# Performance work log

Hardware: AMD Instinct MI355X
Metric: run time of the kernel (lower is better)

Reference implementation:

```python
import jax, jax.numpy as jnp
import numpy as np

BATCH = 4096
FEATURES = 64
VOCAB = 580000
EMB_DIM = 32
MODELS = 512
SEQ_LEN = 128


def _positional_encoding(position, d_model):
    # Faithful to the numpy get_angles: 1/10000^(2*(i//2)/d_model), sin on even, cos on odd.
    pos = jnp.arange(position, dtype=jnp.float32)[:, None]          # [P, 1]
    i = jnp.arange(d_model, dtype=jnp.float32)[None, :]             # [1, D]
    angle_rates = 1.0 / jnp.power(10000.0, (2.0 * jnp.floor(i / 2.0)) / jnp.float32(d_model))
    angles = pos * angle_rates                                      # [P, D]
    even = (jnp.arange(d_model) % 2 == 0)[None, :]
    pe = jnp.where(even, jnp.sin(angles), jnp.cos(angles))
    return pe[None]                                                 # [1, P, D]


def setup_inputs() -> dict:
    key = jax.random.key(0)
    k1, k2, k3 = jax.random.split(key, 3)
    tokens = jax.random.randint(k1, (BATCH, FEATURES), 0, VOCAB, dtype=jnp.int32)
    emb_table = jax.random.normal(k2, (VOCAB, EMB_DIM), dtype=jnp.float32)
    W = jax.random.normal(k3, (FEATURES * EMB_DIM, MODELS), dtype=jnp.float32) * 0.02
    b = jnp.zeros((MODELS,), dtype=jnp.float32)
    return {"tokens": tokens, "emb_table": emb_table, "W": W, "b": b}


def reference(tokens, emb_table, W, b):
    B, F = tokens.shape
    # gather + scale by sqrt(models)
    x = emb_table[tokens] * jnp.sqrt(jnp.float32(MODELS))           # [B, F, E]
    x = x.reshape(B, F * EMB_DIM)                                   # [B, F*E]
    x = x @ W + b                                                   # [B, M]
    # tf.tile(row, [seq_len]) then reshape (seq_len, models) == broadcast over seq axis
    pe = _positional_encoding(SEQ_LEN, MODELS)                      # [1, S, M]
    out = x[:, None, :] + pe[:, :SEQ_LEN, :]                        # [B, S, M]
    return out
```

## Files before the change

### kernel.cpp

```cpp
#include <hip/hip_runtime.h>
#include <math.h>

#define BATCH   4096
#define FEAT    64
#define EMB     32
#define MODELS  512
#define SEQ     128
#define KDIM    (FEAT * EMB)

#define SQRT_MODELS 22.62741699796952f
#define LN10000     9.210340371976184f

typedef __attribute__((ext_vector_type(4))) float    f32x4;
typedef __attribute__((ext_vector_type(8))) short    bf16x8;
typedef __attribute__((ext_vector_type(4))) unsigned int u32x4;

#define WT_BYTES ((size_t)MODELS * KDIM * 2)
#define PE_BYTES ((size_t)SEQ * MODELS * 4)
#define X_BYTES  ((size_t)BATCH * MODELS * 4)
#define WS_NEEDED (WT_BYTES + PE_BYTES + X_BYTES)

__device__ inline unsigned short bf16_rne(float f) {
    unsigned int b = __builtin_bit_cast(unsigned int, f);
    return (unsigned short)((b + 0x7FFFu + ((b >> 16) & 1u)) >> 16);
}

__global__ __launch_bounds__(256)
void prep_wt(const float* __restrict__ W, unsigned short* __restrict__ Wt) {
    __shared__ float t[32][33];
    const int k0 = blockIdx.x * 32;
    const int n0 = blockIdx.y * 32;
    const int tx = threadIdx.x;
    const int ty = threadIdx.y;
    #pragma unroll
    for (int i = 0; i < 4; ++i) {
        const int kk = ty + i * 8;
        t[kk][tx] = W[(size_t)(k0 + kk) * MODELS + n0 + tx] * SQRT_MODELS;
    }
    __syncthreads();
    #pragma unroll
    for (int i = 0; i < 4; ++i) {
        const int nn = ty + i * 8;
        Wt[(size_t)(n0 + nn) * KDIM + k0 + tx] = bf16_rne(t[tx][nn]);
    }
}

__global__ __launch_bounds__(256)
void prep_pe(const float* __restrict__ bias, float* __restrict__ pe) {
    const int idx = blockIdx.x * 256 + threadIdx.x;
    const int s = idx >> 9;
    const int m = idx & (MODELS - 1);
    const float rate = expf(-LN10000 * (float)(2 * (m >> 1)) * (1.0f / 512.0f));
    const float ang  = (float)s * rate;
    pe[idx] = ((m & 1) ? cosf(ang) : sinf(ang)) + bias[m];
}

__global__ __launch_bounds__(256)
void gemm_mfma(const int* __restrict__ tokens, const float* __restrict__ emb,
               const unsigned short* __restrict__ Wt, float* __restrict__ x) {
    const int tid  = threadIdx.x;
    const int wave = tid >> 6;
    const int lane = tid & 63;
    const int ln   = lane & 15;
    const int kg   = lane >> 4;

    const int m_base = blockIdx.y * 16;
    const int n_base = blockIdx.x * 256 + wave * 64;

    const int* trow = tokens + (size_t)(m_base + ln) * FEAT;

    const unsigned short* bptr[4];
    #pragma unroll
    for (int nf = 0; nf < 4; ++nf)
        bptr[nf] = Wt + (size_t)(n_base + nf * 16 + ln) * KDIM + kg * 8;

    f32x4 acc[4] = {f32x4{0,0,0,0}, f32x4{0,0,0,0}, f32x4{0,0,0,0}, f32x4{0,0,0,0}};

    for (int f4 = 0; f4 < FEAT; f4 += 4) {
        const int4 tok4 = *(const int4*)(trow + f4);
        const int toks[4] = {tok4.x, tok4.y, tok4.z, tok4.w};
        #pragma unroll
        for (int j = 0; j < 4; ++j) {
            const int f = f4 + j;
            const float* ea = emb + (size_t)toks[j] * EMB + kg * 8;
            const f32x4 a0 = *(const f32x4*)ea;
            const f32x4 a1 = *(const f32x4*)(ea + 4);
            unsigned int q0, q1, q2, q3;
            asm("v_cvt_pk_bf16_f32 %0, %1, %2" : "=v"(q0) : "v"(a0.x), "v"(a0.y));
            asm("v_cvt_pk_bf16_f32 %0, %1, %2" : "=v"(q1) : "v"(a0.z), "v"(a0.w));
            asm("v_cvt_pk_bf16_f32 %0, %1, %2" : "=v"(q2) : "v"(a1.x), "v"(a1.y));
            asm("v_cvt_pk_bf16_f32 %0, %1, %2" : "=v"(q3) : "v"(a1.z), "v"(a1.w));
            const u32x4 pk = {q0, q1, q2, q3};
            const bf16x8 afrag = __builtin_bit_cast(bf16x8, pk);
            #pragma unroll
            for (int nf = 0; nf < 4; ++nf) {
                const bf16x8 bfrag = *(const bf16x8*)(bptr[nf] + (size_t)f * EMB);
                acc[nf] = __builtin_amdgcn_mfma_f32_16x16x32_bf16(afrag, bfrag, acc[nf], 0, 0, 0);
            }
        }
    }

    #pragma unroll
    for (int nf = 0; nf < 4; ++nf) {
        #pragma unroll
        for (int q = 0; q < 4; ++q) {
            const int r = kg * 4 + q;
            x[(size_t)(m_base + r) * MODELS + n_base + nf * 16 + ln] = acc[nf][q];
        }
    }
}

__global__ __launch_bounds__(256)
void bcast_pe(const float* __restrict__ x, const float* __restrict__ pe,
              float* __restrict__ out) {
    const int tid = threadIdx.x;
    const int m4  = tid & 127;
    const int b   = blockIdx.x * 2 + (tid >> 7);
    const f32x4 xv = *(const f32x4*)(x + (size_t)b * MODELS + m4 * 4);
    const f32x4* pev = (const f32x4*)pe;
    float* ob = out + (size_t)b * SEQ * MODELS + m4 * 4;
    #pragma unroll 4
    for (int s = 0; s < SEQ; ++s) {
        const f32x4 p = pev[s * 128 + m4];
        *(f32x4*)(ob + (size_t)s * MODELS) = xv + p;
    }
}

#define BM 64
#define BN 64
#define BK 32
__global__ __launch_bounds__(256, 2)
void fused_emb_gemm_pe(const int* __restrict__ tokens, const float* __restrict__ emb,
                       const float* __restrict__ W, const float* __restrict__ bias,
                       float* __restrict__ out) {
    __shared__ float As[BK][BM];
    __shared__ float Bs[BK][BN];
    __shared__ float peS[SEQ][BN];
    const int tid  = threadIdx.x;
    const int bn   = blockIdx.x * BN;
    const int brow = blockIdx.y * BM;
    for (int idx = tid; idx < SEQ * BN; idx += 256) {
        const int s  = idx >> 6;
        const int ml = idx & 63;
        const int m  = bn + ml;
        const float rate = expf(-LN10000 * (float)(2 * (m >> 1)) * (1.0f / 512.0f));
        const float ang  = (float)s * rate;
        peS[s][ml] = (m & 1) ? cosf(ang) : sinf(ang);
    }
    float acc[4][4] = {};
    const int tx = tid & 15;
    const int ty = tid >> 4;
    const int lr = tid >> 2;
    const int lj = tid & 3;
    const int bk = tid >> 4;
    const int bc = (tid & 15) * 4;
    for (int kt = 0; kt < FEAT; ++kt) {
        __syncthreads();
        {
            const int tok = tokens[(brow + lr) * FEAT + kt];
            const float* erow = emb + (size_t)tok * EMB + lj * 8;
            const float4 a0 = *(const float4*)(erow);
            const float4 a1 = *(const float4*)(erow + 4);
            const int k0 = lj * 8;
            As[k0 + 0][lr] = a0.x * SQRT_MODELS; As[k0 + 1][lr] = a0.y * SQRT_MODELS;
            As[k0 + 2][lr] = a0.z * SQRT_MODELS; As[k0 + 3][lr] = a0.w * SQRT_MODELS;
            As[k0 + 4][lr] = a1.x * SQRT_MODELS; As[k0 + 5][lr] = a1.y * SQRT_MODELS;
            As[k0 + 6][lr] = a1.z * SQRT_MODELS; As[k0 + 7][lr] = a1.w * SQRT_MODELS;
        }
        {
            const float* w0 = W + (size_t)(kt * 32 + bk) * MODELS + bn + bc;
            const float* w1 = W + (size_t)(kt * 32 + bk + 16) * MODELS + bn + bc;
            *(float4*)&Bs[bk][bc]      = *(const float4*)w0;
            *(float4*)&Bs[bk + 16][bc] = *(const float4*)w1;
        }
        __syncthreads();
        #pragma unroll
        for (int k = 0; k < BK; ++k) {
            const float4 a = *(const float4*)&As[k][ty * 4];
            const float4 b = *(const float4*)&Bs[k][tx * 4];
            acc[0][0] += a.x * b.x; acc[0][1] += a.x * b.y; acc[0][2] += a.x * b.z; acc[0][3] += a.x * b.w;
            acc[1][0] += a.y * b.x; acc[1][1] += a.y * b.y; acc[1][2] += a.y * b.z; acc[1][3] += a.y * b.w;
            acc[2][0] += a.z * b.x; acc[2][1] += a.z * b.y; acc[2][2] += a.z * b.z; acc[2][3] += a.z * b.w;
            acc[3][0] += a.w * b.x; acc[3][1] += a.w * b.y; acc[3][2] += a.w * b.z; acc[3][3] += a.w * b.w;
        }
    }
    {
        const float4 bv = *(const float4*)(bias + bn + tx * 4);
        #pragma unroll
        for (int i = 0; i < 4; ++i) {
            acc[i][0] += bv.x; acc[i][1] += bv.y; acc[i][2] += bv.z; acc[i][3] += bv.w;
        }
    }
    size_t rowbase[4];
    #pragma unroll
    for (int i = 0; i < 4; ++i)
        rowbase[i] = ((size_t)(brow + ty * 4 + i) * SEQ) * MODELS + bn + tx * 4;
    #pragma unroll 4
    for (int s = 0; s < SEQ; ++s) {
        const float4 pv = *(const float4*)&peS[s][tx * 4];
        const size_t soff = (size_t)s * MODELS;
        #pragma unroll
        for (int i = 0; i < 4; ++i) {
            float4 o;
            o.x = acc[i][0] + pv.x; o.y = acc[i][1] + pv.y;
            o.z = acc[i][2] + pv.z; o.w = acc[i][3] + pv.w;
            *(float4*)(out + rowbase[i] + soff) = o;
        }
    }
}

extern "C" void kernel_launch(void* const* d_in, const int* in_sizes, int n_in,
                              void* d_out, int out_size, void* d_ws, size_t ws_size,
                              hipStream_t stream) {
    const int*   tokens = (const int*)d_in[0];
    const float* emb    = (const float*)d_in[1];
    const float* W      = (const float*)d_in[2];
    const float* bias   = (const float*)d_in[3];
    float*       out    = (float*)d_out;

    if (ws_size >= WS_NEEDED) {
        char* w = (char*)d_ws;
        unsigned short* Wt = (unsigned short*)w;
        float* pe = (float*)(w + WT_BYTES);
        float* x  = (float*)(w + WT_BYTES + PE_BYTES);

        prep_wt<<<dim3(KDIM / 32, MODELS / 32), dim3(32, 8), 0, stream>>>(W, Wt);
        prep_pe<<<dim3(SEQ * MODELS / 256), dim3(256), 0, stream>>>(bias, pe);
        gemm_mfma<<<dim3(MODELS / 256, BATCH / 16), dim3(256), 0, stream>>>(tokens, emb, Wt, x);
        bcast_pe<<<dim3(BATCH / 2), dim3(256), 0, stream>>>(x, pe, out);
    } else {
        fused_emb_gemm_pe<<<dim3(MODELS / BN, BATCH / BM), dim3(256), 0, stream>>>(
            tokens, emb, W, bias, out);
    }
}
```

Before: 301.8 us.

## Fuse MFMA embedding GEMM with positional-encoding broadcast store

Merges the GEMM and broadcast kernels into one. Each block computes a 16x128 output tile for two batch tiles, stages it in shared memory, and writes the 128-step broadcast with the PE added directly. This drops the intermediate x buffer write and read plus one kernel launch. In exchange the grid shrinks to 512 blocks and the per-block work is serialized, which may reduce parallelism and overlap on the store-bound broadcast.

```diff
diff --git a/kernel.cpp b/kernel.cpp
--- a/kernel.cpp
+++ b/kernel.cpp
@@ -11,14 +11,13 @@
 #define SQRT_MODELS 22.62741699796952f
 #define LN10000     9.210340371976184f
 
-typedef __attribute__((ext_vector_type(4))) float    f32x4;
-typedef __attribute__((ext_vector_type(8))) short    bf16x8;
+typedef __attribute__((ext_vector_type(4))) float        f32x4;
+typedef __attribute__((ext_vector_type(8))) short        bf16x8;
 typedef __attribute__((ext_vector_type(4))) unsigned int u32x4;
 
 #define WT_BYTES ((size_t)MODELS * KDIM * 2)
 #define PE_BYTES ((size_t)SEQ * MODELS * 4)
-#define X_BYTES  ((size_t)BATCH * MODELS * 4)
-#define WS_NEEDED (WT_BYTES + PE_BYTES + X_BYTES)
+#define WS_NEEDED (WT_BYTES + PE_BYTES)
 
 __device__ inline unsigned short bf16_rne(float f) {
     unsigned int b = __builtin_bit_cast(unsigned int, f);
@@ -55,74 +54,79 @@
     pe[idx] = ((m & 1) ? cosf(ang) : sinf(ang)) + bias[m];
 }
 
+#define TN 128
+#define XS_STRIDE 132
+
 __global__ __launch_bounds__(256)
-void gemm_mfma(const int* __restrict__ tokens, const float* __restrict__ emb,
-               const unsigned short* __restrict__ Wt, float* __restrict__ x) {
+void gemm_bcast(const int* __restrict__ tokens, const float* __restrict__ emb,
+                const unsigned short* __restrict__ Wt, const float* __restrict__ pe,
+                float* __restrict__ out) {
+    __shared__ float xs[16 * XS_STRIDE];
+
     const int tid  = threadIdx.x;
+    const int lane = tid & 63;
     const int wave = tid >> 6;
-    const int lane = tid & 63;
     const int ln   = lane & 15;
     const int kg   = lane >> 4;
 
-    const int m_base = blockIdx.y * 16;
-    const int n_base = blockIdx.x * 256 + wave * 64;
-
-    const int* trow = tokens + (size_t)(m_base + ln) * FEAT;
-
-    const unsigned short* bptr[4];
-    #pragma unroll
-    for (int nf = 0; nf < 4; ++nf)
-        bptr[nf] = Wt + (size_t)(n_base + nf * 16 + ln) * KDIM + kg * 8;
-
-    f32x4 acc[4] = {f32x4{0,0,0,0}, f32x4{0,0,0,0}, f32x4{0,0,0,0}, f32x4{0,0,0,0}};
-
-    for (int f4 = 0; f4 < FEAT; f4 += 4) {
-        const int4 tok4 = *(const int4*)(trow + f4);
-        const int toks[4] = {tok4.x, tok4.y, tok4.z, tok4.w};
-        #pragma unroll
-        for (int j = 0; j < 4; ++j) {
-            const int f = f4 + j;
-            const float* ea = emb + (size_t)toks[j] * EMB + kg * 8;
-            const f32x4 a0 = *(const f32x4*)ea;
-            const f32x4 a1 = *(const f32x4*)(ea + 4);
-            unsigned int q0, q1, q2, q3;
-            asm("v_cvt_pk_bf16_f32 %0, %1, %2" : "=v"(q0) : "v"(a0.x), "v"(a0.y));
-            asm("v_cvt_pk_bf16_f32 %0, %1, %2" : "=v"(q1) : "v"(a0.z), "v"(a0.w));
-            asm("v_cvt_pk_bf16_f32 %0, %1, %2" : "=v"(q2) : "v"(a1.x), "v"(a1.y));
-            asm("v_cvt_pk_bf16_f32 %0, %1, %2" : "=v"(q3) : "v"(a1.z), "v"(a1.w));
-            const u32x4 pk = {q0, q1, q2, q3};
-            const bf16x8 afrag = __builtin_bit_cast(bf16x8, pk);
+    const int n_base = (blockIdx.x & 3) * TN;
+    const int mpair  = blockIdx.x >> 2;
+
+    const int c4 = tid & 31;
+    const int rg = tid >> 5;
+
+    const unsigned short* bbase = Wt + (size_t)(n_base + wave * 32 + ln) * KDIM + kg * 8;
+
+    #pragma unroll 1
+    for (int t = 0; t < 2; ++t) {
+        const int m_base = (mpair * 2 + t) * 16;
+
+        const int* trow = tokens + (size_t)(m_base + ln) * FEAT;
+        f32x4 acc0 = {0, 0, 0, 0}, acc1 = {0, 0, 0, 0};
+
+        for (int f4 = 0; f4 < FEAT; f4 += 4) {
+            const int4 tok4 = *(const int4*)(trow + f4);
+            const int toks[4] = {tok4.x, tok4.y, tok4.z, tok4.w};
             #pragma unroll
-            for (int nf = 0; nf < 4; ++nf) {
-                const bf16x8 bfrag = *(const bf16x8*)(bptr[nf] + (size_t)f * EMB);
-                acc[nf] = __builtin_amdgcn_mfma_f32_16x16x32_bf16(afrag, bfrag, acc[nf], 0, 0, 0);
+            for (int j = 0; j < 4; ++j) {
+                const float* ea = emb + (size_t)toks[j] * EMB + kg * 8;
+                const f32x4 a0 = *(const f32x4*)ea;
+                const f32x4 a1 = *(const f32x4*)(ea + 4);
+                unsigned int q0, q1, q2, q3;
+                asm("v_cvt_pk_bf16_f32 %0, %1, %2" : "=v"(q0) : "v"(a0.x), "v"(a0.y));
+                asm("v_cvt_pk_bf16_f32 %0, %1, %2" : "=v"(q1) : "v"(a0.z), "v"(a0.w));
+                asm("v_cvt_pk_bf16_f32 %0, %1, %2" : "=v"(q2) : "v"(a1.x), "v"(a1.y));
+                asm("v_cvt_pk_bf16_f32 %0, %1, %2" : "=v"(q3) : "v"(a1.z), "v"(a1.w));
+                const u32x4 pk = {q0, q1, q2, q3};
+                const bf16x8 afrag = __builtin_bit_cast(bf16x8, pk);
+                const int f = f4 + j;
+                const bf16x8 bf0 = *(const bf16x8*)(bbase + (size_t)f * EMB);
+                const bf16x8 bf1 = *(const bf16x8*)(bbase + 16 * KDIM + (size_t)f * EMB);
+                acc0 = __builtin_amdgcn_mfma_f32_16x16x32_bf16(afrag, bf0, acc0, 0, 0, 0);
+                acc1 = __builtin_amdgcn_mfma_f32_16x16x32_bf16(afrag, bf1, acc1, 0, 0, 0);
             }
         }
-    }
-
-    #pragma unroll
-    for (int nf = 0; nf < 4; ++nf) {
+
+        __syncthreads();
+
         #pragma unroll
         for (int q = 0; q < 4; ++q) {
-            const int r = kg * 4 + q;
-            x[(size_t)(m_base + r) * MODELS + n_base + nf * 16 + ln] = acc[nf][q];
-        }
-    }
-}
-
-__global__ __launch_bounds__(256)
-void bcast_pe(const float* __restrict__ x, const float* __restrict__ pe,
-              float* __restrict__ out) {
-    const int tid = threadIdx.x;
-    const int m4  = tid & 127;
-    const int b   = blockIdx.x * 2 + (tid >> 7);
-    const f32x4 xv = *(const f32x4*)(x + (size_t)b * MODELS + m4 * 4);
-    const f32x4* pev = (const f32x4*)pe;
-    float* ob = out + (size_t)b * SEQ * MODELS + m4 * 4;
-    #pragma unroll 4
-    for (int s = 0; s < SEQ; ++s) {
-        const f32x4 p = pev[s * 128 + m4];
-        *(f32x4*)(ob + (size_t)s * MODELS) = xv + p;
+            xs[(kg * 4 + q) * XS_STRIDE + wave * 32 + ln]      = acc0[q];
+            xs[(kg * 4 + q) * XS_STRIDE + wave * 32 + 16 + ln] = acc1[q];
+        }
+        __syncthreads();
+
+        const f32x4 x0 = *(const f32x4*)&xs[(rg * 2) * XS_STRIDE + c4 * 4];
+        const f32x4 x1 = *(const f32x4*)&xs[(rg * 2 + 1) * XS_STRIDE + c4 * 4];
+        const float* peb = pe + n_base + c4 * 4;
+        float* ob0 = out + (size_t)(m_base + rg * 2) * SEQ * MODELS + n_base + c4 * 4;
+        float* ob1 = ob0 + (size_t)SEQ * MODELS;
+        #pragma unroll 4
+        for (int s = 0; s < SEQ; ++s) {
+            const f32x4 pv = *(const f32x4*)(peb + (size_t)s * MODELS);
+            *(f32x4*)(ob0 + (size_t)s * MODELS) = x0 + pv;
+            *(f32x4*)(ob1 + (size_t)s * MODELS) = x1 + pv;
+        }
     }
 }
 
@@ -222,12 +226,10 @@
         char* w = (char*)d_ws;
         unsigned short* Wt = (unsigned short*)w;
         float* pe = (float*)(w + WT_BYTES);
-        float* x  = (float*)(w + WT_BYTES + PE_BYTES);
 
         prep_wt<<<dim3(KDIM / 32, MODELS / 32), dim3(32, 8), 0, stream>>>(W, Wt);
         prep_pe<<<dim3(SEQ * MODELS / 256), dim3(256), 0, stream>>>(bias, pe);
-        gemm_mfma<<<dim3(MODELS / 256, BATCH / 16), dim3(256), 0, stream>>>(tokens, emb, Wt, x);
-        bcast_pe<<<dim3(BATCH / 2), dim3(256), 0, stream>>>(x, pe, out);
+        gemm_bcast<<<dim3(512), dim3(256), 0, stream>>>(tokens, emb, Wt, pe, out);
     } else {
         fused_emb_gemm_pe<<<dim3(MODELS / BN, BATCH / BM), dim3(256), 0, stream>>>(
             tokens, emb, W, bias, out);
```

After: 327.6 us. +8.5%, slower.

## Split embedding gather into a bf16 staging kernel and a dense MFMA GEMM

Applied to the files above, without the earlier changes.

Adds a gather kernel that writes the token embeddings as a dense bf16 A matrix into workspace. A separate GEMM then runs over 64x64 block tiles, with each wave computing a 2x2 grid of 16x16 MFMA tiles. The aim is to reuse each A fragment across two N tiles and to get coalesced, contiguous A loads instead of scattered table gathers inside the GEMM. The cost is an extra 16 MB write and read of the staged A matrix, one more launch, and a larger workspace requirement; if the workspace is too small, the old path is used.

```diff
diff --git a/kernel.cpp b/kernel.cpp
--- a/kernel.cpp
+++ b/kernel.cpp
@@ -11,19 +11,31 @@
 #define SQRT_MODELS 22.62741699796952f
 #define LN10000     9.210340371976184f
 
-typedef __attribute__((ext_vector_type(4))) float    f32x4;
-typedef __attribute__((ext_vector_type(8))) short    bf16x8;
+typedef __attribute__((ext_vector_type(4))) float        f32x4;
+typedef __attribute__((ext_vector_type(8))) short        bf16x8;
 typedef __attribute__((ext_vector_type(4))) unsigned int u32x4;
 
-#define WT_BYTES ((size_t)MODELS * KDIM * 2)
-#define PE_BYTES ((size_t)SEQ * MODELS * 4)
-#define X_BYTES  ((size_t)BATCH * MODELS * 4)
-#define WS_NEEDED (WT_BYTES + PE_BYTES + X_BYTES)
+#define WT_BYTES  ((size_t)MODELS * KDIM * 2)
+#define PE_BYTES  ((size_t)SEQ * MODELS * 4)
+#define X_BYTES   ((size_t)BATCH * MODELS * 4)
+#define ABF_BYTES ((size_t)BATCH * KDIM * 2)
+#define WS_MID    (WT_BYTES + PE_BYTES + X_BYTES)
+#define WS_FULL   (WT_BYTES + PE_BYTES + X_BYTES + ABF_BYTES)
 
 __device__ inline unsigned short bf16_rne(float f) {
     unsigned int b = __builtin_bit_cast(unsigned int, f);
     return (unsigned short)((b + 0x7FFFu + ((b >> 16) & 1u)) >> 16);
 }
+
+#define CVT_PK4(pk, v0, v1)                                                     \
+    {                                                                           \
+        unsigned int q0, q1, q2, q3;                                            \
+        asm("v_cvt_pk_bf16_f32 %0, %1, %2" : "=v"(q0) : "v"(v0.x), "v"(v0.y));  \
+        asm("v_cvt_pk_bf16_f32 %0, %1, %2" : "=v"(q1) : "v"(v0.z), "v"(v0.w));  \
+        asm("v_cvt_pk_bf16_f32 %0, %1, %2" : "=v"(q2) : "v"(v1.x), "v"(v1.y));  \
+        asm("v_cvt_pk_bf16_f32 %0, %1, %2" : "=v"(q3) : "v"(v1.z), "v"(v1.w));  \
+        pk = (u32x4){q0, q1, q2, q3};                                           \
+    }
 
 __global__ __launch_bounds__(256)
 void prep_wt(const float* __restrict__ W, unsigned short* __restrict__ Wt) {
@@ -56,6 +68,63 @@
 }
 
 __global__ __launch_bounds__(256)
+void gather_a(const int* __restrict__ tokens, const float* __restrict__ emb,
+              unsigned short* __restrict__ Abf) {
+    const int g    = blockIdx.x * 256 + threadIdx.x;
+    const int fr   = g >> 2;
+    const int part = g & 3;
+    const int tok  = tokens[fr];
+    const float* src = emb + (size_t)tok * EMB + part * 8;
+    const f32x4 v0 = *(const f32x4*)src;
+    const f32x4 v1 = *(const f32x4*)(src + 4);
+    u32x4 pk;
+    CVT_PK4(pk, v0, v1);
+    *(u32x4*)(Abf + (size_t)g * 8) = pk;
+}
+
+__global__ __launch_bounds__(256)
+void gemm_dense(const unsigned short* __restrict__ Abf,
+                const unsigned short* __restrict__ Wt,
+                float* __restrict__ x) {
+    const int tid  = threadIdx.x;
+    const int lane = tid & 63;
+    const int wave = tid >> 6;
+    const int ln   = lane & 15;
+    const int kg   = lane >> 4;
+    const int m0 = blockIdx.y * 64 + (wave >> 1) * 32;
+    const int n0 = blockIdx.x * 64 + (wave & 1) * 32;
+
+    const unsigned short* a0p = Abf + (size_t)(m0 + ln) * KDIM + kg * 8;
+    const unsigned short* a1p = a0p + 16 * KDIM;
+    const unsigned short* b0p = Wt + (size_t)(n0 + ln) * KDIM + kg * 8;
+    const unsigned short* b1p = b0p + 16 * KDIM;
+
+    f32x4 acc00 = {0,0,0,0}, acc01 = {0,0,0,0};
+    f32x4 acc10 = {0,0,0,0}, acc11 = {0,0,0,0};
+
+    #pragma unroll 4
+    for (int k = 0; k < KDIM; k += 32) {
+        const bf16x8 a0 = *(const bf16x8*)(a0p + k);
+        const bf16x8 a1 = *(const bf16x8*)(a1p + k);
+        const bf16x8 b0 = *(const bf16x8*)(b0p + k);
+        const bf16x8 b1 = *(const bf16x8*)(b1p + k);
+        acc00 = __builtin_amdgcn_mfma_f32_16x16x32_bf16(a0, b0, acc00, 0, 0, 0);
+        acc01 = __builtin_amdgcn_mfma_f32_16x16x32_bf16(a0, b1, acc01, 0, 0, 0);
+        acc10 = __builtin_amdgcn_mfma_f32_16x16x32_bf16(a1, b0, acc10, 0, 0, 0);
+        acc11 = __builtin_amdgcn_mfma_f32_16x16x32_bf16(a1, b1, acc11, 0, 0, 0);
+    }
+
+    #pragma unroll
+    for (int q = 0; q < 4; ++q) {
+        const int r = kg * 4 + q;
+        x[(size_t)(m0 + r)      * MODELS + n0 + ln]      = acc00[q];
+        x[(size_t)(m0 + r)      * MODELS + n0 + 16 + ln] = acc01[q];
+        x[(size_t)(m0 + 16 + r) * MODELS + n0 + ln]      = acc10[q];
+        x[(size_t)(m0 + 16 + r) * MODELS + n0 + 16 + ln] = acc11[q];
+    }
+}
+
+__global__ __launch_bounds__(256)
 void gemm_mfma(const int* __restrict__ tokens, const float* __restrict__ emb,
                const unsigned short* __restrict__ Wt, float* __restrict__ x) {
     const int tid  = threadIdx.x;
@@ -63,19 +132,14 @@
     const int lane = tid & 63;
     const int ln   = lane & 15;
     const int kg   = lane >> 4;
-
     const int m_base = blockIdx.y * 16;
     const int n_base = blockIdx.x * 256 + wave * 64;
-
     const int* trow = tokens + (size_t)(m_base + ln) * FEAT;
-
     const unsigned short* bptr[4];
     #pragma unroll
     for (int nf = 0; nf < 4; ++nf)
         bptr[nf] = Wt + (size_t)(n_base + nf * 16 + ln) * KDIM + kg * 8;
-
     f32x4 acc[4] = {f32x4{0,0,0,0}, f32x4{0,0,0,0}, f32x4{0,0,0,0}, f32x4{0,0,0,0}};
-
     for (int f4 = 0; f4 < FEAT; f4 += 4) {
         const int4 tok4 = *(const int4*)(trow + f4);
         const int toks[4] = {tok4.x, tok4.y, tok4.z, tok4.w};
@@ -85,12 +149,8 @@
             const float* ea = emb + (size_t)toks[j] * EMB + kg * 8;
             const f32x4 a0 = *(const f32x4*)ea;
             const f32x4 a1 = *(const f32x4*)(ea + 4);
-            unsigned int q0, q1, q2, q3;
-            asm("v_cvt_pk_bf16_f32 %0, %1, %2" : "=v"(q0) : "v"(a0.x), "v"(a0.y));
-            asm("v_cvt_pk_bf16_f32 %0, %1, %2" : "=v"(q1) : "v"(a0.z), "v"(a0.w));
-            asm("v_cvt_pk_bf16_f32 %0, %1, %2" : "=v"(q2) : "v"(a1.x), "v"(a1.y));
-            asm("v_cvt_pk_bf16_f32 %0, %1, %2" : "=v"(q3) : "v"(a1.z), "v"(a1.w));
-            const u32x4 pk = {q0, q1, q2, q3};
+            u32x4 pk;
+            CVT_PK4(pk, a0, a1);
             const bf16x8 afrag = __builtin_bit_cast(bf16x8, pk);
             #pragma unroll
             for (int nf = 0; nf < 4; ++nf) {
@@ -99,15 +159,11 @@
             }
         }
     }
-
-    #pragma unroll
-    for (int nf = 0; nf < 4; ++nf) {
-        #pragma unroll
-        for (int q = 0; q < 4; ++q) {
-            const int r = kg * 4 + q;
-            x[(size_t)(m_base + r) * MODELS + n_base + nf * 16 + ln] = acc[nf][q];
-        }
-    }
+    #pragma unroll
+    for (int nf = 0; nf < 4; ++nf)
+        #pragma unroll
+        for (int q = 0; q < 4; ++q)
+            x[(size_t)(m_base + kg * 4 + q) * MODELS + n_base + nf * 16 + ln] = acc[nf][q];
 }
 
 __global__ __launch_bounds__(256)
@@ -218,7 +274,19 @@
     const float* bias   = (const float*)d_in[3];
     float*       out    = (float*)d_out;
 
-    if (ws_size >= WS_NEEDED) {
+    if (ws_size >= WS_FULL) {
+        char* w = (char*)d_ws;
+        unsigned short* Wt  = (unsigned short*)w;
+        float*          pe  = (float*)(w + WT_BYTES);
+        float*          x   = (float*)(w + WT_BYTES + PE_BYTES);
+        unsigned short* Abf = (unsigned short*)(w + WT_BYTES + PE_BYTES + X_BYTES);
+
+        prep_wt<<<dim3(KDIM / 32, MODELS / 32), dim3(32, 8), 0, stream>>>(W, Wt);
+        prep_pe<<<dim3(SEQ * MODELS / 256), dim3(256), 0, stream>>>(bias, pe);
+        gather_a<<<dim3(BATCH * KDIM / 8 / 256), dim3(256), 0, stream>>>(tokens, emb, Abf);
+        gemm_dense<<<dim3(MODELS / 64, BATCH / 64), dim3(256), 0, stream>>>(Abf, Wt, x);
+        bcast_pe<<<dim3(BATCH / 2), dim3(256), 0, stream>>>(x, pe, out);
+    } else if (ws_size >= WS_MID) {
         char* w = (char*)d_ws;
         unsigned short* Wt = (unsigned short*)w;
         float* pe = (float*)(w + WT_BYTES);
```

Result: faster. 278.2 us (-7.8%).

## Fuse GEMM with PE broadcast via LDS and merge prep kernels

Applied to the files above, without the earlier changes.

Merges the weight-transpose and PE-table prep kernels into one launch. Fuses the embedding GEMM with the sequence broadcast: each 512-thread block computes all 512 output columns for 16 batch rows, stages the result in shared memory, then writes the 128-step broadcast with nontemporal stores. This removes the intermediate x buffer round trip and two kernel launches. In exchange the GEMM grid shrinks to 256 blocks and each block does a long store-bound tail.

```diff
diff --git a/kernel.cpp b/kernel.cpp
--- a/kernel.cpp
+++ b/kernel.cpp
@@ -11,64 +11,79 @@
 #define SQRT_MODELS 22.62741699796952f
 #define LN10000     9.210340371976184f
 
-typedef __attribute__((ext_vector_type(4))) float    f32x4;
-typedef __attribute__((ext_vector_type(8))) short    bf16x8;
+typedef __attribute__((ext_vector_type(4))) float        f32x4;
+typedef __attribute__((ext_vector_type(8))) short        bf16x8;
 typedef __attribute__((ext_vector_type(4))) unsigned int u32x4;
 
-#define WT_BYTES ((size_t)MODELS * KDIM * 2)
-#define PE_BYTES ((size_t)SEQ * MODELS * 4)
-#define X_BYTES  ((size_t)BATCH * MODELS * 4)
-#define WS_NEEDED (WT_BYTES + PE_BYTES + X_BYTES)
+#define WT_BYTES  ((size_t)MODELS * KDIM * 2)
+#define PE_BYTES  ((size_t)SEQ * MODELS * 4)
+#define WS_NEEDED (WT_BYTES + PE_BYTES)
 
 __device__ inline unsigned short bf16_rne(float f) {
     unsigned int b = __builtin_bit_cast(unsigned int, f);
     return (unsigned short)((b + 0x7FFFu + ((b >> 16) & 1u)) >> 16);
 }
 
+#define CVT_PK4(pk, v0, v1)                                                     \
+    {                                                                           \
+        unsigned int q0, q1, q2, q3;                                            \
+        asm("v_cvt_pk_bf16_f32 %0, %1, %2" : "=v"(q0) : "v"(v0.x), "v"(v0.y));  \
+        asm("v_cvt_pk_bf16_f32 %0, %1, %2" : "=v"(q1) : "v"(v0.z), "v"(v0.w));  \
+        asm("v_cvt_pk_bf16_f32 %0, %1, %2" : "=v"(q2) : "v"(v1.x), "v"(v1.y));  \
+        asm("v_cvt_pk_bf16_f32 %0, %1, %2" : "=v"(q3) : "v"(v1.z), "v"(v1.w));  \
+        pk = (u32x4){q0, q1, q2, q3};                                           \
+    }
+
 __global__ __launch_bounds__(256)
-void prep_wt(const float* __restrict__ W, unsigned short* __restrict__ Wt) {
-    __shared__ float t[32][33];
-    const int k0 = blockIdx.x * 32;
-    const int n0 = blockIdx.y * 32;
-    const int tx = threadIdx.x;
-    const int ty = threadIdx.y;
-    #pragma unroll
-    for (int i = 0; i < 4; ++i) {
-        const int kk = ty + i * 8;
-        t[kk][tx] = W[(size_t)(k0 + kk) * MODELS + n0 + tx] * SQRT_MODELS;
-    }
-    __syncthreads();
-    #pragma unroll
-    for (int i = 0; i < 4; ++i) {
-        const int nn = ty + i * 8;
-        Wt[(size_t)(n0 + nn) * KDIM + k0 + tx] = bf16_rne(t[tx][nn]);
-    }
-}
-
-__global__ __launch_bounds__(256)
-void prep_pe(const float* __restrict__ bias, float* __restrict__ pe) {
-    const int idx = blockIdx.x * 256 + threadIdx.x;
-    const int s = idx >> 9;
-    const int m = idx & (MODELS - 1);
-    const float rate = expf(-LN10000 * (float)(2 * (m >> 1)) * (1.0f / 512.0f));
-    const float ang  = (float)s * rate;
-    pe[idx] = ((m & 1) ? cosf(ang) : sinf(ang)) + bias[m];
-}
-
-__global__ __launch_bounds__(256)
-void gemm_mfma(const int* __restrict__ tokens, const float* __restrict__ emb,
-               const unsigned short* __restrict__ Wt, float* __restrict__ x) {
+void prep(const float* __restrict__ W, const float* __restrict__ bias,
+          unsigned short* __restrict__ Wt, float* __restrict__ pe) {
+    const int bx  = blockIdx.x;
+    const int tid = threadIdx.x;
+    if (bx < 1024) {
+        __shared__ float t[32][33];
+        const int k0 = (bx & 63) * 32;
+        const int n0 = (bx >> 6) * 32;
+        const int tx = tid & 31;
+        const int ty = tid >> 5;
+        #pragma unroll
+        for (int i = 0; i < 4; ++i) {
+            const int kk = ty + i * 8;
+            t[kk][tx] = W[(size_t)(k0 + kk) * MODELS + n0 + tx] * SQRT_MODELS;
+        }
+        __syncthreads();
+        #pragma unroll
+        for (int i = 0; i < 4; ++i) {
+            const int nn = ty + i * 8;
+            Wt[(size_t)(n0 + nn) * KDIM + k0 + tx] = bf16_rne(t[tx][nn]);
+        }
+    } else {
+        const int idx = (bx - 1024) * 256 + tid;
+        const int s = idx >> 9;
+        const int m = idx & (MODELS - 1);
+        const float rate = expf(-LN10000 * (float)(2 * (m >> 1)) * (1.0f / 512.0f));
+        const float ang  = (float)s * rate;
+        pe[idx] = ((m & 1) ? cosf(ang) : sinf(ang)) + bias[m];
+    }
+}
+
+#define XS_STRIDE 516
+
+__global__ __launch_bounds__(512)
+void gemm_bcast(const int* __restrict__ tokens, const float* __restrict__ emb,
+                const unsigned short* __restrict__ Wt, const float* __restrict__ pe,
+                float* __restrict__ out) {
+    __shared__ float xs[16 * XS_STRIDE];
+
     const int tid  = threadIdx.x;
     const int wave = tid >> 6;
     const int lane = tid & 63;
     const int ln   = lane & 15;
     const int kg   = lane >> 4;
 
-    const int m_base = blockIdx.y * 16;
-    const int n_base = blockIdx.x * 256 + wave * 64;
-
-    const int* trow = tokens + (size_t)(m_base + ln) * FEAT;
-
+    const int m0     = blockIdx.x * 16;
+    const int n_base = wave * 64;
+
+    const int* trow = tokens + (size_t)(m0 + ln) * FEAT;
     const unsigned short* bptr[4];
     #pragma unroll
     for (int nf = 0; nf < 4; ++nf)
@@ -81,17 +96,13 @@
         const int toks[4] = {tok4.x, tok4.y, tok4.z, tok4.w};
         #pragma unroll
         for (int j = 0; j < 4; ++j) {
-            const int f = f4 + j;
             const float* ea = emb + (size_t)toks[j] * EMB + kg * 8;
             const f32x4 a0 = *(const f32x4*)ea;
             const f32x4 a1 = *(const f32x4*)(ea + 4);
-            unsigned int q0, q1, q2, q3;
-            asm("v_cvt_pk_bf16_f32 %0, %1, %2" : "=v"(q0) : "v"(a0.x), "v"(a0.y));
-            asm("v_cvt_pk_bf16_f32 %0, %1, %2" : "=v"(q1) : "v"(a0.z), "v"(a0.w));
-            asm("v_cvt_pk_bf16_f32 %0, %1, %2" : "=v"(q2) : "v"(a1.x), "v"(a1.y));
-            asm("v_cvt_pk_bf16_f32 %0, %1, %2" : "=v"(q3) : "v"(a1.z), "v"(a1.w));
-            const u32x4 pk = {q0, q1, q2, q3};
+            u32x4 pk;
+            CVT_PK4(pk, a0, a1);
             const bf16x8 afrag = __builtin_bit_cast(bf16x8, pk);
+            const int f = f4 + j;
             #pragma unroll
             for (int nf = 0; nf < 4; ++nf) {
                 const bf16x8 bfrag = *(const bf16x8*)(bptr[nf] + (size_t)f * EMB);
@@ -101,28 +112,31 @@
     }
 
     #pragma unroll
-    for (int nf = 0; nf < 4; ++nf) {
-        #pragma unroll
-        for (int q = 0; q < 4; ++q) {
-            const int r = kg * 4 + q;
-            x[(size_t)(m_base + r) * MODELS + n_base + nf * 16 + ln] = acc[nf][q];
-        }
-    }
-}
-
-__global__ __launch_bounds__(256)
-void bcast_pe(const float* __restrict__ x, const float* __restrict__ pe,
-              float* __restrict__ out) {
-    const int tid = threadIdx.x;
-    const int m4  = tid & 127;
-    const int b   = blockIdx.x * 2 + (tid >> 7);
-    const f32x4 xv = *(const f32x4*)(x + (size_t)b * MODELS + m4 * 4);
-    const f32x4* pev = (const f32x4*)pe;
-    float* ob = out + (size_t)b * SEQ * MODELS + m4 * 4;
-    #pragma unroll 4
+    for (int nf = 0; nf < 4; ++nf)
+        #pragma unroll
+        for (int q = 0; q < 4; ++q)
+            xs[(kg * 4 + q) * XS_STRIDE + n_base + nf * 16 + ln] = acc[nf][q];
+
+    __syncthreads();
+
+    const int r = tid >> 5;
+    const int c = (tid & 31) * 4;
+
+    f32x4 xv[4];
+    #pragma unroll
+    for (int p = 0; p < 4; ++p)
+        xv[p] = *(const f32x4*)&xs[r * XS_STRIDE + p * 128 + c];
+
+    float* ob = out + (size_t)(m0 + r) * SEQ * MODELS;
+    const float* peb = pe;
+    #pragma unroll 2
     for (int s = 0; s < SEQ; ++s) {
-        const f32x4 p = pev[s * 128 + m4];
-        *(f32x4*)(ob + (size_t)s * MODELS) = xv + p;
+        const size_t so = (size_t)s * MODELS;
+        #pragma unroll
+        for (int p = 0; p < 4; ++p) {
+            const f32x4 pv = *(const f32x4*)(peb + so + p * 128 + c);
+            __builtin_nontemporal_store(xv[p] + pv, (f32x4*)(ob + so + p * 128 + c));
+        }
     }
 }
 
@@ -221,13 +235,10 @@
     if (ws_size >= WS_NEEDED) {
         char* w = (char*)d_ws;
         unsigned short* Wt = (unsigned short*)w;
-        float* pe = (float*)(w + WT_BYTES);
-        float* x  = (float*)(w + WT_BYTES + PE_BYTES);
-
-        prep_wt<<<dim3(KDIM / 32, MODELS / 32), dim3(32, 8), 0, stream>>>(W, Wt);
-        prep_pe<<<dim3(SEQ * MODELS / 256), dim3(256), 0, stream>>>(bias, pe);
-        gemm_mfma<<<dim3(MODELS / 256, BATCH / 16), dim3(256), 0, stream>>>(tokens, emb, Wt, x);
-        bcast_pe<<<dim3(BATCH / 2), dim3(256), 0, stream>>>(x, pe, out);
+        float*          pe = (float*)(w + WT_BYTES);
+
+        prep<<<dim3(1024 + 256), dim3(256), 0, stream>>>(W, bias, Wt, pe);
+        gemm_bcast<<<dim3(BATCH / 16), dim3(512), 0, stream>>>(tokens, emb, Wt, pe, out);
     } else {
         fused_emb_gemm_pe<<<dim3(MODELS / BN, BATCH / BM), dim3(256), 0, stream>>>(
             tokens, emb, W, bias, out);
```

New measurement: 336.6 us. 1.12x slower.
